# Performance work log

Hardware: AMD Instinct MI355X
Metric: run time of the kernel (lower is better)

The kernel has to match this reference:

```python
import jax, jax.numpy as jnp
import numpy as np

D_MODEL, D_STATE, D_CONV, D_INNER = 256, 16, 4, 512
N_LAYERS, VOCAB = 2, 256
THR, MIN_P, MAX_P = 0.5, 1, 8
LOG_VOCAB = float(np.log(VOCAB))


def _rmsnorm(x, w):
    eps = jnp.finfo(x.dtype).eps
    return x * jax.lax.rsqrt(jnp.mean(x * x, axis=-1, keepdims=True) + eps) * w


def _mamba_block(x, in_w, cw, cb, xp_w, dtw, dtb, a_log, d, ow, nw):
    res = x
    x_in, z = jnp.split(x @ in_w, 2, axis=-1)  # (b,s,d_inner) each
    # causal depthwise conv: torch pads both sides d_conv-1 then slices [:s] == left-pad only
    xc = jax.lax.conv_general_dilated(
        x_in.transpose(0, 2, 1), cw, (1,), [(D_CONV - 1, 0)],
        feature_group_count=D_INNER, dimension_numbers=('NCH', 'OIH', 'NCH'))
    xc = jax.nn.silu((xc + cb[None, :, None]).transpose(0, 2, 1))  # (b,s,d_inner)
    Bmat, _C = jnp.split(xc @ xp_w, 2, axis=-1)  # (b,s,d_state); C unused as in original
    dt = jax.nn.softplus(xc @ dtw + dtb)         # (b,s,d_inner)
    A = -jnp.exp(a_log)                          # (d_inner,d_state)
    dA = jnp.exp(A[None, None] * dt[..., None])  # (b,s,d_inner,d_state)
    # y = sum_n dA * (dt*B*x) = dt*x * einsum(dA, B) ; avoids a second 4-D temp
    y = dt * xc * jnp.einsum('bsdn,bsn->bsd', dA, Bmat) + d * xc
    y = (y * jax.nn.silu(z)) @ ow
    return _rmsnorm(y + res, nw)


def _entropy_model(bytes_input, embed_w, in_proj_w, conv_w, conv_b, x_proj_w,
                   dt_w, dt_b, A_log, D_param, out_w, norm_w, head_w):
    x = embed_w[bytes_input]
    for l in range(N_LAYERS):
        x = _mamba_block(x, in_proj_w[l], conv_w[l], conv_b[l], x_proj_w[l],
                         dt_w[l], dt_b[l], A_log[l], D_param[l], out_w[l], norm_w[l])
    logp = jax.nn.log_softmax(x @ head_w, axis=-1)
    return -jnp.sum(jnp.exp(logp) * logp, axis=-1) / LOG_VOCAB  # (b,s) normalized entropy


def _boundaries(entropy):
    B = entropy.shape[0]
    def step(size, e):
        nb = ((e > THR) & (size >= MIN_P)) | (size >= MAX_P)
        return jnp.where(nb, 1, size + 1), nb
    _, nb = jax.lax.scan(step, jnp.ones((B,), jnp.int32), entropy[:, 1:].T)
    return jnp.concatenate([jnp.ones((B, 1), bool), nb.T], axis=1)  # (b,s)


def _patch(byte_embeddings, byte_to_patch):
    # mean pooling over patches; padded to static max of seq_len patches
    B, S, _ = byte_embeddings.shape
    seg = jax.vmap(lambda v, s: jax.ops.segment_sum(v, s, num_segments=S))
    sums = seg(byte_embeddings, byte_to_patch)                       # (b,S,d)
    counts = seg(jnp.ones((B, S), byte_embeddings.dtype), byte_to_patch)  # (b,S)
    patch_emb = sums / jnp.maximum(counts, 1.0)[..., None]
    return patch_emb, counts.astype(jnp.int32)


def setup_inputs() -> dict:
    key = jax.random.key(0)
    k = jax.random.split(key, 12)
    B, S = 8, 2048
    s = 0.05
    return {
        'bytes_input': jax.random.randint(k[0], (B, S), 0, VOCAB),
        'byte_embeddings': jax.random.normal(k[1], (B, S, D_MODEL), jnp.float32),
        'embed_w': jax.random.normal(k[2], (VOCAB, D_MODEL)) * s,
        'in_proj_w': jax.random.normal(k[3], (N_LAYERS, D_MODEL, 2 * D_INNER)) * s,
        'conv_w': jax.random.normal(k[4], (N_LAYERS, D_INNER, 1, D_CONV)) * s,
        'conv_b': jax.random.normal(k[5], (N_LAYERS, D_INNER)) * s,
        'x_proj_w': jax.random.normal(k[6], (N_LAYERS, D_INNER, 2 * D_STATE)) * s,
        'dt_w': jax.random.normal(k[7], (N_LAYERS, D_INNER, D_INNER)) * s,
        'dt_b': jax.random.normal(k[8], (N_LAYERS, D_INNER)) * s,
        'A_log': jax.random.normal(k[9], (N_LAYERS, D_INNER, D_STATE)),
        'D_param': jnp.ones((N_LAYERS, D_INNER)),
        'out_w': jax.random.normal(k[10], (N_LAYERS, D_INNER, D_MODEL)) * s,
        'norm_w': jnp.ones((N_LAYERS, D_MODEL)),
        'head_w': jax.random.normal(k[11], (D_MODEL, VOCAB)) * s,
    }


def reference(bytes_input, byte_embeddings, embed_w, in_proj_w, conv_w, conv_b,
              x_proj_w, dt_w, dt_b, A_log, D_param, out_w, norm_w, head_w):
    entropy = _entropy_model(bytes_input, embed_w, in_proj_w, conv_w, conv_b,
                             x_proj_w, dt_w, dt_b, A_log, D_param, out_w, norm_w, head_w)
    is_boundary = _boundaries(entropy)
    byte_to_patch = jnp.cumsum(is_boundary.astype(jnp.int32), axis=1) - 1  # (b,s)
    patch_embeddings, patch_lengths = _patch(byte_embeddings, byte_to_patch)
    return patch_embeddings, patch_lengths, byte_to_patch
```

## Files before the change

kernel.cpp:

```cpp
#include <hip/hip_runtime.h>
#include <hip/hip_bf16.h>
#include <math.h>

#define BB 8
#define SS 2048
#define TT (BB * SS)
#define DM 256
#define DI 512
#define DSTATE 16
#define DCONV 4
#define NLAYERS 2
#define VOCAB 256
#define LOG_VOCAB 5.545177444479562f
#define RMS_EPS 1.1920929e-07f
#define LOG2E 1.4426950408889634f
#define LN2 0.6931471805599453f
#define THR_ 0.5f

#define TW 32
#define XBST 264
#define XST 520
#define BMST 20
#define VST 260
#define HST3 264
#define XBS_BYTES 25344
#define VST_OFF 25344
#define HTS_OFF 25344
#define RMSP_OFF 42240
#define RED_OFF 61744

typedef __attribute__((ext_vector_type(8))) __bf16 bf16x8;
typedef __attribute__((ext_vector_type(4))) __bf16 bf16x4;
typedef __attribute__((ext_vector_type(2))) __bf16 bf16x2;
typedef __attribute__((ext_vector_type(4))) float f32x4;

__device__ __forceinline__ float fexp(float x) { return __builtin_amdgcn_exp2f(x * LOG2E); }
__device__ __forceinline__ float fexp2(float x) { return __builtin_amdgcn_exp2f(x); }
__device__ __forceinline__ float flog(float x) { return __builtin_amdgcn_logf(x) * LN2; }
__device__ __forceinline__ float frcp(float x) { return __builtin_amdgcn_rcpf(x); }
__device__ __forceinline__ float fsigmoid(float x) { return frcp(1.f + fexp(-x)); }
__device__ __forceinline__ float fsoftplus(float x) {
  return fmaxf(x, 0.f) + flog(1.f + fexp(-fabsf(x)));
}

__device__ __forceinline__ size_t pkidx(int n, int k, int K) {
  return ((size_t)(n >> 4) * (K >> 5) + (k >> 5)) * 512 +
         ((((k >> 3) & 3) * 16 + (n & 15)) * 8) + (k & 7);
}

#define WT_BLOCKS 352
#define PW_BLOCKS (WT_BLOCKS + 16)

__global__ __launch_bounds__(256) void prep_wtrans(
    const float* __restrict__ in_proj_w, __hip_bfloat16* __restrict__ inWt,
    const float* __restrict__ dt_w, __hip_bfloat16* __restrict__ dtWt,
    const float* __restrict__ out_w, __hip_bfloat16* __restrict__ oWt,
    const float* __restrict__ head_w, __hip_bfloat16* __restrict__ headWt,
    const float* __restrict__ x_proj_w, __hip_bfloat16* __restrict__ xpWt,
    const float* __restrict__ A_log, float* __restrict__ A2) {
  __shared__ float tile[64][65];
  int bid = blockIdx.x;
  int tid = threadIdx.x;
  if (bid >= WT_BLOCKS) {
    int i = (bid - WT_BLOCKS) * 256 + tid;
    f32x4 a = *(const f32x4*)(A_log + i * 4);
    f32x4 o;
#pragma unroll
    for (int j = 0; j < 4; ++j) o[j] = -fexp(a[j]) * LOG2E;
    *(f32x4*)(A2 + i * 4) = o;
    return;
  }
  const float* src;
  __hip_bfloat16* dst;
  int K, N, kt, nt, nw = 64;
  if (bid < 128) {
    int l = bid >> 6, r = bid & 63;
    src = in_proj_w + (size_t)l * 262144; dst = inWt + (size_t)l * 262144;
    K = 256; N = 1024; kt = r >> 4; nt = r & 15;
  } else if (bid < 256) {
    int i = bid - 128; int l = i >> 6, r = i & 63;
    src = dt_w + (size_t)l * 262144; dst = dtWt + (size_t)l * 262144;
    K = 512; N = 512; kt = r >> 3; nt = r & 7;
  } else if (bid < 320) {
    int i = bid - 256; int l = i >> 5, r = i & 31;
    src = out_w + (size_t)l * 131072; dst = oWt + (size_t)l * 131072;
    K = 512; N = 256; kt = r >> 2; nt = r & 3;
  } else if (bid < 336) {
    int r = bid - 320;
    src = head_w; dst = headWt;
    K = 256; N = 256; kt = r >> 2; nt = r & 3;
  } else {
    int i = bid - 336; int l = i >> 3, r = i & 7;
    src = x_proj_w + (size_t)l * 16384; dst = xpWt + (size_t)l * 16384;
    K = 512; N = 32; kt = r; nt = 0; nw = 32;
  }
  int k0 = kt * 64, n0 = nt * 64;
  if (nw == 64) {
    int r0 = tid >> 4, c4 = (tid & 15) * 4;
#pragma unroll
    for (int rr = 0; rr < 4; ++rr) {
      int r = rr * 16 + r0;
      f32x4 v = *(const f32x4*)(src + (size_t)(k0 + r) * N + n0 + c4);
      tile[r][c4] = v[0]; tile[r][c4 + 1] = v[1]; tile[r][c4 + 2] = v[2]; tile[r][c4 + 3] = v[3];
    }
    __syncthreads();
    int n = tid >> 2, kc = (tid & 3) * 16;
#pragma unroll
    for (int cc = 0; cc < 2; ++cc) {
      int k = kc + cc * 8;
      bf16x8 o;
#pragma unroll
      for (int j = 0; j < 8; ++j) o[j] = (__bf16)tile[k + j][n];
      *(bf16x8*)((__bf16*)dst + pkidx(n0 + n, k0 + k, K)) = o;
    }
  } else {
    int r0 = tid >> 3, c4 = (tid & 7) * 4;
#pragma unroll
    for (int rr = 0; rr < 2; ++rr) {
      int r = rr * 32 + r0;
      f32x4 v = *(const f32x4*)(src + (size_t)(k0 + r) * N + c4);
      tile[r][c4] = v[0]; tile[r][c4 + 1] = v[1]; tile[r][c4 + 2] = v[2]; tile[r][c4 + 3] = v[3];
    }
    __syncthreads();
    int n = tid >> 3, kc = (tid & 7) * 8;
    bf16x8 o;
#pragma unroll
    for (int j = 0; j < 8; ++j) o[j] = (__bf16)tile[kc + j][n];
    *(bf16x8*)((__bf16*)dst + pkidx(n, k0 + kc, K)) = o;
  }
}

template <bool DOHEAD, bool EMBED>
__global__ __launch_bounds__(512, 4) void mamba_fused(
    const __hip_bfloat16* __restrict__ xbin,
    __hip_bfloat16* __restrict__ xbout,
    const int* __restrict__ byts,
    const float* __restrict__ embw,
    const __bf16* __restrict__ inW,
    const __bf16* __restrict__ dtW,
    const __bf16* __restrict__ oW,
    const __bf16* __restrict__ xpW,
    const float* __restrict__ cw, const float* __restrict__ cb,
    const float* __restrict__ A2, const float* __restrict__ dtb,
    const float* __restrict__ Dp, const float* __restrict__ nw,
    const __bf16* __restrict__ hW, float* __restrict__ ent) {
  extern __shared__ char smem[];
  __bf16* xbs = (__bf16*)smem;
  __bf16* xcs = (__bf16*)(smem + XBS_BYTES);
  float* Bms = (float*)(smem + XBS_BYTES + 35 * XST * 2);

  int tid = threadIdx.x;
  int lane = tid & 63;
  int w = tid >> 6;
  int quad = lane >> 4;
  int l15 = lane & 15;
  int t0 = blockIdx.x * TW;
  int s0 = t0 & (SS - 1);

#pragma unroll
  for (int it = 0; it < 3; ++it) {
    int idx = it * 512 + tid;
    int r = idx >> 5, c8 = (idx & 31) * 8;
    int tok = t0 - 16 + r;
    if (tok < 0) tok = 0;
    if constexpr (EMBED) {
      const float* srcp = embw + (size_t)byts[tok] * DM + c8;
      f32x4 v0 = *(const f32x4*)srcp;
      f32x4 v1 = *(const f32x4*)(srcp + 4);
      bf16x8 ob;
#pragma unroll
      for (int j = 0; j < 4; ++j) { ob[j] = (__bf16)v0[j]; ob[4 + j] = (__bf16)v1[j]; }
      *(bf16x8*)(xbs + r * XBST + c8) = ob;
    } else {
      *(bf16x8*)(xbs + r * XBST + c8) =
          *(const bf16x8*)((const __bf16*)xbin + (size_t)tok * DM + c8);
    }
  }
  __syncthreads();

  int wn64 = w * 64;
#pragma unroll 1
  for (int cth = 0; cth < 2; ++cth) {
    const __bf16* bp[2];
#pragma unroll
    for (int ni = 0; ni < 2; ++ni)
      bp[ni] = inW + (size_t)(w * 4 + cth * 2 + ni) * 8 * 512 + lane * 8;
    f32x4 ga[3][2] = {};
    bf16x8 bnx0[2], bnx1[2];
#pragma unroll
    for (int ni = 0; ni < 2; ++ni) {
      bnx0[ni] = *(const bf16x8*)(bp[ni]);
      bnx1[ni] = *(const bf16x8*)(bp[ni] + 512);
    }
#pragma unroll
    for (int kk = 0; kk < 8; ++kk) {
      int k0 = kk * 32;
      bf16x8 bcur[2];
#pragma unroll
      for (int ni = 0; ni < 2; ++ni) { bcur[ni] = bnx0[ni]; bnx0[ni] = bnx1[ni]; }
      if (kk < 6) {
#pragma unroll
        for (int ni = 0; ni < 2; ++ni)
          bnx1[ni] = *(const bf16x8*)(bp[ni] + (size_t)(kk + 2) * 512);
      }
      bf16x8 af[3];
#pragma unroll
      for (int rt = 0; rt < 3; ++rt)
        af[rt] = *(const bf16x8*)(xbs + (rt * 16 + l15) * XBST + k0 + quad * 8);
#pragma unroll
      for (int rt = 0; rt < 3; ++rt)
#pragma unroll
        for (int ni = 0; ni < 2; ++ni)
          ga[rt][ni] = __builtin_amdgcn_mfma_f32_16x16x32_bf16(af[rt], bcur[ni], ga[rt][ni], 0, 0, 0);
    }
#pragma unroll
    for (int rt = 0; rt < 3; ++rt)
#pragma unroll
      for (int ni = 0; ni < 2; ++ni)
#pragma unroll
        for (int rg = 0; rg < 4; ++rg) {
          int grow = rt * 16 + quad * 4 + rg;
          if (grow >= 13)
            xcs[(grow - 13) * XST + wn64 + cth * 32 + ni * 16 + l15] = (__bf16)ga[rt][ni][rg];
        }
  }
  __syncthreads();

  {
    int d = tid;
    float wv[4];
#pragma unroll
    for (int k = 0; k < 4; ++k) wv[k] = cw[d * 4 + k];
    float b = cb[d];
    float h0 = 0, h1 = 0, h2 = 0;
    if (s0 > 0) {
      h0 = (float)xcs[0 * XST + d];
      h1 = (float)xcs[1 * XST + d];
      h2 = (float)xcs[2 * XST + d];
    }
#pragma unroll 4
    for (int s = 0; s < TW; ++s) {
      float c = (float)xcs[(s + 3) * XST + d];
      float a = b + wv[0] * h0 + wv[1] * h1 + wv[2] * h2 + wv[3] * c;
      xcs[(s + 3) * XST + d] = (__bf16)(a * fsigmoid(a));
      h0 = h1; h1 = h2; h2 = c;
    }
  }
  __syncthreads();

  if (w < 2) {
    f32x4 bacc = {};
#pragma unroll
    for (int kk = 0; kk < 16; ++kk) {
      bf16x8 a = *(const bf16x8*)(xcs + (w * 16 + l15 + 3) * XST + kk * 32 + quad * 8);
      bf16x8 bb = *(const bf16x8*)(xpW + (size_t)kk * 512 + lane * 8);
      bacc = __builtin_amdgcn_mfma_f32_16x16x32_bf16(a, bb, bacc, 0, 0, 0);
    }
#pragma unroll
    for (int rg = 0; rg < 4; ++rg)
      Bms[(w * 16 + quad * 4 + rg) * BMST + l15] = bacc[rg];
  }

  int dbase = w * 64;
  f32x4 acc[2][4] = {};
  {
    const __bf16* dtp[4];
#pragma unroll
    for (int ni = 0; ni < 4; ++ni)
      dtp[ni] = dtW + (size_t)(w * 4 + ni) * 16 * 512 + lane * 8;
    bf16x8 bnx0[4], bnx1[4];
#pragma unroll
    for (int ni = 0; ni < 4; ++ni) {
      bnx0[ni] = *(const bf16x8*)(dtp[ni]);
      bnx1[ni] = *(const bf16x8*)(dtp[ni] + 512);
    }
#pragma unroll
    for (int kk = 0; kk < 16; ++kk) {
      int k0 = kk * 32;
      bf16x8 bcur[4];
#pragma unroll
      for (int ni = 0; ni < 4; ++ni) { bcur[ni] = bnx0[ni]; bnx0[ni] = bnx1[ni]; }
      if (kk < 14) {
#pragma unroll
        for (int ni = 0; ni < 4; ++ni)
          bnx1[ni] = *(const bf16x8*)(dtp[ni] + (size_t)(kk + 2) * 512);
      }
      bf16x8 af[2];
#pragma unroll
      for (int mi = 0; mi < 2; ++mi)
        af[mi] = *(const bf16x8*)(xcs + (mi * 16 + l15 + 3) * XST + k0 + quad * 8);
#pragma unroll
      for (int mi = 0; mi < 2; ++mi)
#pragma unroll
        for (int ni = 0; ni < 4; ++ni)
          acc[mi][ni] = __builtin_amdgcn_mfma_f32_16x16x32_bf16(af[mi], bcur[ni], acc[mi][ni], 0, 0, 0);
    }
  }

  bf16x4 zsave[2][2][2];
#pragma unroll
  for (int cth = 0; cth < 2; ++cth) {
    const __bf16* bp[2];
#pragma unroll
    for (int ni = 0; ni < 2; ++ni)
      bp[ni] = inW + (size_t)(32 + w * 4 + cth * 2 + ni) * 8 * 512 + lane * 8;
    f32x4 gz[2][2] = {};
    bf16x8 bnx0[2], bnx1[2];
#pragma unroll
    for (int ni = 0; ni < 2; ++ni) {
      bnx0[ni] = *(const bf16x8*)(bp[ni]);
      bnx1[ni] = *(const bf16x8*)(bp[ni] + 512);
    }
#pragma unroll
    for (int kk = 0; kk < 8; ++kk) {
      int k0 = kk * 32;
      bf16x8 bcur[2];
#pragma unroll
      for (int ni = 0; ni < 2; ++ni) { bcur[ni] = bnx0[ni]; bnx0[ni] = bnx1[ni]; }
      if (kk < 6) {
#pragma unroll
        for (int ni = 0; ni < 2; ++ni)
          bnx1[ni] = *(const bf16x8*)(bp[ni] + (size_t)(kk + 2) * 512);
      }
      bf16x8 af[2];
#pragma unroll
      for (int rt = 0; rt < 2; ++rt)
        af[rt] = *(const bf16x8*)(xbs + ((16 + rt * 16) + l15) * XBST + k0 + quad * 8);
#pragma unroll
      for (int rt = 0; rt < 2; ++rt)
#pragma unroll
        for (int ni = 0; ni < 2; ++ni)
          gz[rt][ni] = __builtin_amdgcn_mfma_f32_16x16x32_bf16(af[rt], bcur[ni], gz[rt][ni], 0, 0, 0);
    }
#pragma unroll
    for (int rt = 0; rt < 2; ++rt)
#pragma unroll
      for (int ni = 0; ni < 2; ++ni)
#pragma unroll
        for (int rg = 0; rg < 4; ++rg)
          zsave[cth][rt][ni][rg] = (__bf16)gz[rt][ni][rg];
  }
  __syncthreads();

#pragma unroll
  for (int ni = 0; ni < 4; ++ni) {
    int d = dbase + ni * 16 + l15;
    float dtbv = dtb[d];
    float dpv = Dp[d];
    const f32x4* ar = (const f32x4*)(A2 + d * DSTATE);
    f32x4 av[4];
#pragma unroll
    for (int q = 0; q < 4; ++q) av[q] = ar[q];
#pragma unroll
    for (int mi = 0; mi < 2; ++mi) {
#pragma unroll
      for (int rg = 0; rg < 4; ++rg) {
        int tl = mi * 16 + quad * 4 + rg;
        const f32x4* br = (const f32x4*)(Bms + tl * BMST);
        float dt = fsoftplus(acc[mi][ni][rg] + dtbv);
        float s = 0.f;
#pragma unroll
        for (int q = 0; q < 4; ++q) {
          f32x4 bq = br[q];
#pragma unroll
          for (int j = 0; j < 4; ++j) s += fexp2(av[q][j] * dt) * bq[j];
        }
        float xcv = (float)xcs[(tl + 3) * XST + d];
        float y = dt * xcv * s + dpv * xcv;
        float zf = (float)zsave[ni >> 1][mi][ni & 1][rg];
        xcs[(tl + 3) * XST + d] = (__bf16)(y * zf * fsigmoid(zf));
      }
    }
  }
  __syncthreads();

  int wn = w * 32;
  f32x4 oacc[2][2] = {};
  {
    const __bf16* op[2];
#pragma unroll
    for (int ni = 0; ni < 2; ++ni)
      op[ni] = oW + (size_t)(w * 2 + ni) * 16 * 512 + lane * 8;
    bf16x8 onx0[2], onx1[2];
#pragma unroll
    for (int ni = 0; ni < 2; ++ni) {
      onx0[ni] = *(const bf16x8*)(op[ni]);
      onx1[ni] = *(const bf16x8*)(op[ni] + 512);
    }
#pragma unroll
    for (int kk = 0; kk < 16; ++kk) {
      int k0 = kk * 32;
      bf16x8 ocur[2];
#pragma unroll
      for (int ni = 0; ni < 2; ++ni) { ocur[ni] = onx0[ni]; onx0[ni] = onx1[ni]; }
      if (kk < 14) {
#pragma unroll
        for (int ni = 0; ni < 2; ++ni)
          onx1[ni] = *(const bf16x8*)(op[ni] + (size_t)(kk + 2) * 512);
      }
      bf16x8 af[2];
#pragma unroll
      for (int mi = 0; mi < 2; ++mi)
        af[mi] = *(const bf16x8*)(xcs + (mi * 16 + l15 + 3) * XST + k0 + quad * 8);
#pragma unroll
      for (int mi = 0; mi < 2; ++mi)
#pragma unroll
        for (int ni = 0; ni < 2; ++ni)
          oacc[mi][ni] = __builtin_amdgcn_mfma_f32_16x16x32_bf16(af[mi], ocur[ni], oacc[mi][ni], 0, 0, 0);
    }
  }
  __syncthreads();

  if constexpr (!DOHEAD) {
    float* vst = (float*)(smem + VST_OFF);
#pragma unroll
    for (int mi = 0; mi < 2; ++mi)
#pragma unroll
      for (int ni = 0; ni < 2; ++ni)
#pragma unroll
        for (int rg = 0; rg < 4; ++rg) {
          int tl = mi * 16 + quad * 4 + rg;
          vst[tl * VST + wn + ni * 16 + l15] = oacc[mi][ni][rg];
        }
    __syncthreads();

    int row = tid >> 4;
    int seg = tid & 15;
    float vv[4][4];
    float sq = 0.f;
#pragma unroll
    for (int j4 = 0; j4 < 4; ++j4) {
      int c = j4 * 64 + seg * 4;
      bf16x4 rv = *(const bf16x4*)(xbs + (16 + row) * XBST + c);
#pragma unroll
      for (int j = 0; j < 4; ++j) {
        float v = vst[row * VST + c + j] + (float)rv[j];
        vv[j4][j] = v;
        sq += v * v;
      }
    }
    sq += __shfl_xor(sq, 1);
    sq += __shfl_xor(sq, 2);
    sq += __shfl_xor(sq, 4);
    sq += __shfl_xor(sq, 8);
    float r = rsqrtf(sq * (1.f / DM) + RMS_EPS);
    __hip_bfloat16* xbw = xbout + (size_t)(t0 + row) * DM;
#pragma unroll
    for (int j4 = 0; j4 < 4; ++j4) {
      int c = j4 * 64 + seg * 4;
      f32x4 nv = *(const f32x4*)(nw + c);
      bf16x4 ob;
#pragma unroll
      for (int j = 0; j < 4; ++j)
        ob[j] = (__bf16)(vv[j4][j] * r * nv[j]);
      *(bf16x4*)(xbw + c) = ob;
    }
  } else {
    __bf16* hts = (__bf16*)(smem + HTS_OFF);
    float* rmsp = (float*)(smem + RMSP_OFF);
    float vv[2][2][4];
#pragma unroll
    for (int mi = 0; mi < 2; ++mi) {
#pragma unroll
      for (int rg = 0; rg < 4; ++rg) {
        int tl = mi * 16 + quad * 4 + rg;
        float sqp = 0.f;
#pragma unroll
        for (int ni = 0; ni < 2; ++ni) {
          float rv = (float)xbs[(16 + tl) * XBST + wn + ni * 16 + l15];
          float v = oacc[mi][ni][rg] + rv;
          vv[mi][ni][rg] = v;
          sqp += v * v;
        }
        sqp += __shfl_xor(sqp, 1);
        sqp += __shfl_xor(sqp, 2);
        sqp += __shfl_xor(sqp, 4);
        sqp += __shfl_xor(sqp, 8);
        if (l15 == 0) rmsp[tl * 8 + w] = sqp;
      }
    }
    __syncthreads();
#pragma unroll
    for (int mi = 0; mi < 2; ++mi) {
#pragma unroll
      for (int rg = 0; rg < 4; ++rg) {
        int tl = mi * 16 + quad * 4 + rg;
        float tot = 0.f;
#pragma unroll
        for (int ww = 0; ww < 8; ++ww) tot += rmsp[tl * 8 + ww];
        float r = rsqrtf(tot * (1.f / DM) + RMS_EPS);
#pragma unroll
        for (int ni = 0; ni < 2; ++ni) {
          int c = wn + ni * 16 + l15;
          hts[tl * HST3 + c] = (__bf16)(vv[mi][ni][rg] * r * nw[c]);
        }
      }
    }
    __syncthreads();

    float* red = (float*)(smem + RED_OFF);
    int wv = w * 32;
    f32x4 hacc[2][2] = {};
#pragma unroll
    for (int kk = 0; kk < 8; ++kk) {
      int k0 = kk * 32;
      bf16x8 b0 = *(const bf16x8*)(hW + ((size_t)(w * 2) * 8 + kk) * 512 + lane * 8);
      bf16x8 b1 = *(const bf16x8*)(hW + ((size_t)(w * 2 + 1) * 8 + kk) * 512 + lane * 8);
      bf16x8 a0 = *(const bf16x8*)(hts + l15 * HST3 + k0 + quad * 8);
      bf16x8 a1 = *(const bf16x8*)(hts + (16 + l15) * HST3 + k0 + quad * 8);
      hacc[0][0] = __builtin_amdgcn_mfma_f32_16x16x32_bf16(a0, b0, hacc[0][0], 0, 0, 0);
      hacc[0][1] = __builtin_amdgcn_mfma_f32_16x16x32_bf16(a0, b1, hacc[0][1], 0, 0, 0);
      hacc[1][0] = __builtin_amdgcn_mfma_f32_16x16x32_bf16(a1, b0, hacc[1][0], 0, 0, 0);
      hacc[1][1] = __builtin_amdgcn_mfma_f32_16x16x32_bf16(a1, b1, hacc[1][1], 0, 0, 0);
    }
#pragma unroll
    for (int mi = 0; mi < 2; ++mi) {
#pragma unroll
      for (int rg = 0; rg < 4; ++rg) {
        float l0 = hacc[mi][0][rg], l1 = hacc[mi][1][rg];
        float e0 = fexp(l0), e1 = fexp(l1);
        float s = e0 + e1;
        float u = e0 * l0 + e1 * l1;
        s += __shfl_xor(s, 1); u += __shfl_xor(u, 1);
        s += __shfl_xor(s, 2); u += __shfl_xor(u, 2);
        s += __shfl_xor(s, 4); u += __shfl_xor(u, 4);
        s += __shfl_xor(s, 8); u += __shfl_xor(u, 8);
        if (l15 == 0) {
          int tl = mi * 16 + quad * 4 + rg;
          red[(tl * 8 + w) * 2] = s;
          red[(tl * 8 + w) * 2 + 1] = u;
        }
      }
    }
    __syncthreads();
    if (tid < 32) {
      float s = 0.f, u = 0.f;
#pragma unroll
      for (int ww = 0; ww < 8; ++ww) {
        s += red[(tid * 8 + ww) * 2];
        u += red[(tid * 8 + ww) * 2 + 1];
      }
      ent[t0 + tid] = (flog(s) - u * frcp(s)) * (1.f / LOG_VOCAB);
    }
  }
}

__global__ __launch_bounds__(256) void scan_kernel(
    const float* __restrict__ ent, float* __restrict__ btp_out,
    int* __restrict__ pstart, int* __restrict__ npatch) {
  __shared__ int sh[256];
  int b = blockIdx.x, t = threadIdx.x;
  int sbase = t * 8;
  f32x4 e0 = *(const f32x4*)(ent + (size_t)b * SS + sbase);
  f32x4 e1 = *(const f32x4*)(ent + (size_t)b * SS + sbase + 4);
  float e[8] = {e0[0], e0[1], e0[2], e0[3], e1[0], e1[1], e1[2], e1[3]};
  int la = -1;
  unsigned cbits = 0;
#pragma unroll
  for (int j = 0; j < 8; ++j) {
    int s = sbase + j;
    bool cb = (s == 0) || (e[j] > THR_);
    if (cb) { la = s; cbits |= 1u << j; }
  }
  sh[t] = la;
  __syncthreads();
  int run = la;
  for (int off = 1; off < 256; off <<= 1) {
    int other = (t >= off) ? sh[t - off] : -1;
    __syncthreads();
    run = max(run, other);
    sh[t] = run;
    __syncthreads();
  }
  int anchor = (t > 0) ? sh[t - 1] : -1;
  unsigned bits = 0;
#pragma unroll
  for (int j = 0; j < 8; ++j) {
    int s = sbase + j;
    bool cb = (cbits >> j) & 1u;
    bool bnd;
    if (cb) { bnd = true; anchor = s; }
    else bnd = ((s - anchor) & 7) == 0;
    bits |= (unsigned)bnd << j;
  }
  int cnt = __popc(bits);
  __syncthreads();
  sh[t] = cnt;
  __syncthreads();
  int runc = cnt;
  for (int off = 1; off < 256; off <<= 1) {
    int other = (t >= off) ? sh[t - off] : 0;
    __syncthreads();
    runc += other;
    sh[t] = runc;
    __syncthreads();
  }
  if (t == 255) npatch[b] = runc;
  int btp = (runc - cnt) - 1;
#pragma unroll
  for (int j = 0; j < 8; ++j) {
    int s = sbase + j;
    if ((bits >> j) & 1u) { ++btp; pstart[b * SS + btp] = s; }
    btp_out[b * SS + s] = (float)btp;
  }
}

__global__ __launch_bounds__(256) void patch_kernel(
    const float* __restrict__ bemb, const int* __restrict__ pstart,
    const int* __restrict__ npatch, float* __restrict__ pe_out,
    float* __restrict__ plen_out) {
  int bp8 = blockIdx.x;
  int b = bp8 >> 8;
  int p0 = (bp8 & 255) * 8;
  int t = threadIdx.x;
  int g = t >> 5;
  int t32 = t & 31;
  int p = p0 + g;
  int np = npatch[b];
  size_t outbase = ((size_t)b * SS + p) * DM + t32 * 8;
  if (p >= np) {
    f32x4 z = {0.f, 0.f, 0.f, 0.f};
    *(f32x4*)(pe_out + outbase) = z;
    *(f32x4*)(pe_out + outbase + 4) = z;
    if (t32 == 0) plen_out[b * SS + p] = 0.f;
    return;
  }
  int start = pstart[b * SS + p];
  int end = (p + 1 < np) ? pstart[b * SS + p + 1] : SS;
  f32x4 a0 = {0.f, 0.f, 0.f, 0.f}, a1 = {0.f, 0.f, 0.f, 0.f};
  for (int r = start; r < end; ++r) {
    const float* row = bemb + ((size_t)b * SS + r) * DM + t32 * 8;
    f32x4 v0 = *(const f32x4*)row;
    f32x4 v1 = *(const f32x4*)(row + 4);
#pragma unroll
    for (int j = 0; j < 4; ++j) { a0[j] += v0[j]; a1[j] += v1[j]; }
  }
  float inv = frcp((float)(end - start));
#pragma unroll
  for (int j = 0; j < 4; ++j) { a0[j] *= inv; a1[j] *= inv; }
  *(f32x4*)(pe_out + outbase) = a0;
  *(f32x4*)(pe_out + outbase + 4) = a1;
  if (t32 == 0) plen_out[b * SS + p] = (float)(end - start);
}

extern "C" void kernel_launch(void* const* d_in, const int* in_sizes, int n_in,
                              void* d_out, int out_size, void* d_ws, size_t ws_size,
                              hipStream_t stream) {
  const int* bytes = (const int*)d_in[0];
  const float* bemb = (const float*)d_in[1];
  const float* embed_w = (const float*)d_in[2];
  const float* in_proj_w = (const float*)d_in[3];
  const float* conv_w = (const float*)d_in[4];
  const float* conv_b = (const float*)d_in[5];
  const float* x_proj_w = (const float*)d_in[6];
  const float* dt_w = (const float*)d_in[7];
  const float* dt_b = (const float*)d_in[8];
  const float* A_log = (const float*)d_in[9];
  const float* D_param = (const float*)d_in[10];
  const float* out_w = (const float*)d_in[11];
  const float* norm_w = (const float*)d_in[12];
  const float* head_w = (const float*)d_in[13];

  float* out = (float*)d_out;
  float* pe_out = out;
  float* plen_out = out + (size_t)TT * DM;
  float* btp_out = plen_out + TT;

  char* wsb = (char*)d_ws;
  size_t off = 0;
  auto alloc = [&](size_t bytes_) -> void* {
    void* p = wsb + off;
    off += (bytes_ + 255) & ~(size_t)255;
    return p;
  };
  float* A2 = (float*)alloc((size_t)NLAYERS * DI * DSTATE * 4);
  __hip_bfloat16* xb1 = (__hip_bfloat16*)alloc((size_t)TT * DM * 2);
  float* ent = (float*)alloc((size_t)TT * 4);
  int* pstart = (int*)alloc((size_t)TT * 4);
  int* npatch = (int*)alloc(256);
  __hip_bfloat16* inWt = (__hip_bfloat16*)alloc((size_t)NLAYERS * 2 * DI * DM * 2);
  __hip_bfloat16* dtWt = (__hip_bfloat16*)alloc((size_t)NLAYERS * DI * DI * 2);
  __hip_bfloat16* oWt = (__hip_bfloat16*)alloc((size_t)NLAYERS * DM * DI * 2);
  __hip_bfloat16* xpWt = (__hip_bfloat16*)alloc((size_t)NLAYERS * 32 * DI * 2);
  __hip_bfloat16* headWt = (__hip_bfloat16*)alloc((size_t)VOCAB * DM * 2);

  prep_wtrans<<<PW_BLOCKS, 256, 0, stream>>>(
      in_proj_w, inWt, dt_w, dtWt, out_w, oWt, head_w, headWt,
      x_proj_w, xpWt, A_log, A2);

  size_t fused_lds = (size_t)XBS_BYTES + (size_t)35 * XST * 2 + (size_t)TW * BMST * 4;
  mamba_fused<false, true><<<TT / TW, 512, fused_lds, stream>>>(
      nullptr, xb1, bytes, embed_w,
      (const __bf16*)inWt, (const __bf16*)dtWt, (const __bf16*)oWt,
      (const __bf16*)xpWt,
      conv_w, conv_b, A2, dt_b, D_param, norm_w, nullptr, nullptr);

  mamba_fused<true, false><<<TT / TW, 512, fused_lds, stream>>>(
      xb1, nullptr, nullptr, nullptr,
      (const __bf16*)(inWt + (size_t)1 * 2 * DI * DM),
      (const __bf16*)(dtWt + (size_t)1 * DI * DI),
      (const __bf16*)(oWt + (size_t)1 * DM * DI),
      (const __bf16*)(xpWt + (size_t)1 * 32 * DI),
      conv_w + (size_t)1 * DI * DCONV, conv_b + (size_t)1 * DI,
      A2 + (size_t)1 * DI * DSTATE, dt_b + (size_t)1 * DI,
      D_param + (size_t)1 * DI, norm_w + (size_t)1 * DM,
      (const __bf16*)headWt, ent);

  scan_kernel<<<BB, 256, 0, stream>>>(ent, btp_out, pstart, npatch);

  patch_kernel<<<TT / 8, 256, 0, stream>>>(bemb, pstart, npatch, pe_out, plen_out);
}
```

Measured before the change: 215.5 us.

## Load conv halo rows from global directly and shrink LDS footprint

The 16-token causal-conv halo rows are no longer staged in shared memory. Each lane now reads its halo row straight from global memory (embedding table or previous layer output) into registers, prefetched one k-step ahead and fed into the first MFMA row tile. The token tile in LDS shrinks from 48 to 32 rows, and the LDS regions are repacked so the Bms buffer aliases the xcs region, bringing the total from about 64 KB to about 53 KB. This should let a third 512-thread block fit per CU. The cost is extra uncoalesced global loads for the halo, and the Bms/xcs aliasing is only correct if their lifetimes never overlap.

Result: slower. 226.5 us (+5.1%).

```diff
diff --git a/kernel.cpp b/kernel.cpp
--- a/kernel.cpp
+++ b/kernel.cpp
@@ -23,11 +23,14 @@
 #define BMST 20
 #define VST 260
 #define HST3 264
-#define XBS_BYTES 25344
-#define VST_OFF 25344
-#define HTS_OFF 25344
-#define RMSP_OFF 42240
-#define RED_OFF 61744
+#define XBS32_BYTES 16896
+#define XCS_OFF 16896
+#define BMS_OFF 16896
+#define VST_OFF 16896
+#define HTS_OFF 16896
+#define RMSP_OFF 33792
+#define RED_OFF 34816
+#define LDS_TOTAL 53296
 
 typedef __attribute__((ext_vector_type(8))) __bf16 bf16x8;
 typedef __attribute__((ext_vector_type(4))) __bf16 bf16x4;
@@ -146,8 +149,8 @@
     const __bf16* __restrict__ hW, float* __restrict__ ent) {
   extern __shared__ char smem[];
   __bf16* xbs = (__bf16*)smem;
-  __bf16* xcs = (__bf16*)(smem + XBS_BYTES);
-  float* Bms = (float*)(smem + XBS_BYTES + 35 * XST * 2);
+  __bf16* xcs = (__bf16*)(smem + XCS_OFF);
+  float* Bms = (float*)(smem + BMS_OFF);
 
   int tid = threadIdx.x;
   int lane = tid & 63;
@@ -158,11 +161,10 @@
   int s0 = t0 & (SS - 1);
 
 #pragma unroll
-  for (int it = 0; it < 3; ++it) {
+  for (int it = 0; it < 2; ++it) {
     int idx = it * 512 + tid;
     int r = idx >> 5, c8 = (idx & 31) * 8;
-    int tok = t0 - 16 + r;
-    if (tok < 0) tok = 0;
+    int tok = t0 + r;
     if constexpr (EMBED) {
       const float* srcp = embw + (size_t)byts[tok] * DM + c8;
       f32x4 v0 = *(const f32x4*)srcp;
@@ -178,6 +180,25 @@
   }
   __syncthreads();
 
+  int htok = t0 - 16 + l15;
+  if (htok < 0) htok = 0;
+  const float* hrowf = nullptr;
+  const __bf16* hrowb = nullptr;
+  if constexpr (EMBED) hrowf = embw + (size_t)byts[htok] * DM;
+  else hrowb = (const __bf16*)xbin + (size_t)htok * DM;
+  auto ldhalo = [&](int kcol) {
+    bf16x8 r;
+    if constexpr (EMBED) {
+      f32x4 h0 = *(const f32x4*)(hrowf + kcol + quad * 8);
+      f32x4 h1 = *(const f32x4*)(hrowf + kcol + quad * 8 + 4);
+#pragma unroll
+      for (int j = 0; j < 4; ++j) { r[j] = (__bf16)h0[j]; r[4 + j] = (__bf16)h1[j]; }
+    } else {
+      r = *(const bf16x8*)(hrowb + kcol + quad * 8);
+    }
+    return r;
+  };
+
   int wn64 = w * 64;
 #pragma unroll 1
   for (int cth = 0; cth < 2; ++cth) {
@@ -192,6 +213,7 @@
       bnx0[ni] = *(const bf16x8*)(bp[ni]);
       bnx1[ni] = *(const bf16x8*)(bp[ni] + 512);
     }
+    bf16x8 af0nx = ldhalo(0);
 #pragma unroll
     for (int kk = 0; kk < 8; ++kk) {
       int k0 = kk * 32;
@@ -203,15 +225,16 @@
         for (int ni = 0; ni < 2; ++ni)
           bnx1[ni] = *(const bf16x8*)(bp[ni] + (size_t)(kk + 2) * 512);
       }
-      bf16x8 af[3];
-#pragma unroll
-      for (int rt = 0; rt < 3; ++rt)
-        af[rt] = *(const bf16x8*)(xbs + (rt * 16 + l15) * XBST + k0 + quad * 8);
-#pragma unroll
-      for (int rt = 0; rt < 3; ++rt)
-#pragma unroll
-        for (int ni = 0; ni < 2; ++ni)
-          ga[rt][ni] = __builtin_amdgcn_mfma_f32_16x16x32_bf16(af[rt], bcur[ni], ga[rt][ni], 0, 0, 0);
+      bf16x8 af0 = af0nx;
+      if (kk < 7) af0nx = ldhalo(k0 + 32);
+      bf16x8 af1 = *(const bf16x8*)(xbs + (l15)*XBST + k0 + quad * 8);
+      bf16x8 af2 = *(const bf16x8*)(xbs + (16 + l15) * XBST + k0 + quad * 8);
+#pragma unroll
+      for (int ni = 0; ni < 2; ++ni) {
+        ga[0][ni] = __builtin_amdgcn_mfma_f32_16x16x32_bf16(af0, bcur[ni], ga[0][ni], 0, 0, 0);
+        ga[1][ni] = __builtin_amdgcn_mfma_f32_16x16x32_bf16(af1, bcur[ni], ga[1][ni], 0, 0, 0);
+        ga[2][ni] = __builtin_amdgcn_mfma_f32_16x16x32_bf16(af2, bcur[ni], ga[2][ni], 0, 0, 0);
+      }
     }
 #pragma unroll
     for (int rt = 0; rt < 3; ++rt)
@@ -325,7 +348,7 @@
       bf16x8 af[2];
 #pragma unroll
       for (int rt = 0; rt < 2; ++rt)
-        af[rt] = *(const bf16x8*)(xbs + ((16 + rt * 16) + l15) * XBST + k0 + quad * 8);
+        af[rt] = *(const bf16x8*)(xbs + (rt * 16 + l15) * XBST + k0 + quad * 8);
 #pragma unroll
       for (int rt = 0; rt < 2; ++rt)
 #pragma unroll
@@ -431,7 +454,7 @@
 #pragma unroll
     for (int j4 = 0; j4 < 4; ++j4) {
       int c = j4 * 64 + seg * 4;
-      bf16x4 rv = *(const bf16x4*)(xbs + (16 + row) * XBST + c);
+      bf16x4 rv = *(const bf16x4*)(xbs + row * XBST + c);
 #pragma unroll
       for (int j = 0; j < 4; ++j) {
         float v = vst[row * VST + c + j] + (float)rv[j];
@@ -467,7 +490,7 @@
         float sqp = 0.f;
 #pragma unroll
         for (int ni = 0; ni < 2; ++ni) {
-          float rv = (float)xbs[(16 + tl) * XBST + wn + ni * 16 + l15];
+          float rv = (float)xbs[tl * XBST + wn + ni * 16 + l15];
           float v = oacc[mi][ni][rg] + rv;
           vv[mi][ni][rg] = v;
           sqp += v * v;
@@ -499,7 +522,6 @@
     __syncthreads();
 
     float* red = (float*)(smem + RED_OFF);
-    int wv = w * 32;
     f32x4 hacc[2][2] = {};
 #pragma unroll
     for (int kk = 0; kk < 8; ++kk) {
@@ -688,14 +710,13 @@
       in_proj_w, inWt, dt_w, dtWt, out_w, oWt, head_w, headWt,
       x_proj_w, xpWt, A_log, A2);
 
-  size_t fused_lds = (size_t)XBS_BYTES + (size_t)35 * XST * 2 + (size_t)TW * BMST * 4;
-  mamba_fused<false, true><<<TT / TW, 512, fused_lds, stream>>>(
+  mamba_fused<false, true><<<TT / TW, 512, LDS_TOTAL, stream>>>(
       nullptr, xb1, bytes, embed_w,
       (const __bf16*)inWt, (const __bf16*)dtWt, (const __bf16*)oWt,
       (const __bf16*)xpWt,
       conv_w, conv_b, A2, dt_b, D_param, norm_w, nullptr, nullptr);
 
-  mamba_fused<true, false><<<TT / TW, 512, fused_lds, stream>>>(
+  mamba_fused<true, false><<<TT / TW, 512, LDS_TOTAL, stream>>>(
       xb1, nullptr, nullptr, nullptr,
       (const __bf16*)(inWt + (size_t)1 * 2 * DI * DM),
       (const __bf16*)(dtWt + (size_t)1 * DI * DI),
```
